# Optimization experiments

Hardware: AMD Instinct MI355X
Metric: run time of the kernel (lower is better)

Reference implementation:

```python
import jax, jax.numpy as jnp
import numpy as np

B, D, N, H, K = 8192, 1024, 4096, 8, 4
T, DECAY, STEPS = 100.0, 0.001, 3


def setup_inputs() -> dict:
    key = jax.random.key(0)
    ks = jax.random.split(key, 16)
    rn = lambda k, sh, s=0.02: jax.random.normal(k, sh, jnp.float32) * s
    return {
        'query': jax.random.normal(ks[0], (B, D), jnp.float32),
        'wm': jax.random.normal(ks[1], (B, D), jnp.float32),
        'keys': jax.random.normal(ks[2], (N, D), jnp.float32) * 0.1,
        'values': jax.random.normal(ks[3], (N, D), jnp.float32) * 0.1,
        'last_access': jax.random.uniform(ks[4], (N,), jnp.float32) * T,
        'importance': jnp.ones((N,), jnp.float32),
        'consolid': jnp.ones((N,), jnp.float32),
        'emo_tags': jax.random.uniform(ks[5], (N, 8), jnp.float32),
        'active': jnp.ones((N,), jnp.float32),
        'in_proj_w': rn(ks[6], (3 * D, D)), 'in_proj_b': jnp.zeros((3 * D,), jnp.float32),
        'out_w': rn(ks[7], (D, D)), 'out_b': jnp.zeros((D,), jnp.float32),
        'msg_w1': rn(ks[8], (D, 2 * D)), 'msg_b1': jnp.zeros((D,), jnp.float32),
        'msg_ln_g': jnp.ones((D,), jnp.float32), 'msg_ln_b': jnp.zeros((D,), jnp.float32),
        'msg_w2': rn(ks[9], (D, D)), 'msg_b2': jnp.zeros((D,), jnp.float32),
        'gru_wih': rn(ks[10], (3 * D, D)), 'gru_whh': rn(ks[11], (3 * D, D)),
        'gru_bih': jnp.zeros((3 * D,), jnp.float32), 'gru_bhh': jnp.zeros((3 * D,), jnp.float32),
        'rsn_w1': rn(ks[12], (D, D)), 'rsn_b1': jnp.zeros((D,), jnp.float32),
        'rsn_ln_g': jnp.ones((D,), jnp.float32), 'rsn_ln_b': jnp.zeros((D,), jnp.float32),
        'rsn_w2': rn(ks[13], (D, D)), 'rsn_b2': jnp.zeros((D,), jnp.float32),
        'top_k': K,
    }


def _ln(x, g, b):
    m = x.mean(-1, keepdims=True)
    v = ((x - m) ** 2).mean(-1, keepdims=True)
    return (x - m) / jnp.sqrt(v + 1e-5) * g + b


def reference(query, wm, keys, values, last_access, importance, consolid, emo_tags, active,
              in_proj_w, in_proj_b, out_w, out_b,
              msg_w1, msg_b1, msg_ln_g, msg_ln_b, msg_w2, msg_b2,
              gru_wih, gru_whh, gru_bih, gru_bhh,
              rsn_w1, rsn_b1, rsn_ln_g, rsn_ln_b, rsn_w2, rsn_b2, top_k):
    sg = jax.lax.stop_gradient
    # --- schema retrieve: cosine sim + forgetting-decay + boosts + topk softmax gather ---
    qn = query / jnp.maximum(jnp.linalg.norm(query, axis=-1, keepdims=True), 1e-8)
    kn = keys / jnp.maximum(jnp.linalg.norm(keys, axis=-1, keepdims=True), 1e-8)
    sims = qn @ kn.T  # [B, N]
    forget = sg(jnp.exp(-DECAY * (T - last_access)))
    boost = sg(emo_tags.sum(-1) * 0.1 + importance * 0.2 + jnp.log1p(consolid) * 0.1)
    scores = (sims * forget + boost) * sg(active)
    top_s, top_i = jax.lax.top_k(scores, top_k)  # [B, K]
    w = jax.nn.softmax(top_s, axis=-1)
    schema = jnp.einsum('bk,bkd->bd', w, values[top_i])  # [B, D]

    # --- GraphReasoner: 3 steps of 2-token MHA + msg_net + GRUCell ---
    dh = D // H
    scale = 1.0 / np.sqrt(dh).astype(np.float32)

    def mha(x):  # x [B, 2, D]
        qkv = x @ in_proj_w.T + in_proj_b
        q, k, v = jnp.split(qkv, 3, axis=-1)
        q = q.reshape(-1, 2, H, dh); k = k.reshape(-1, 2, H, dh); v = v.reshape(-1, 2, H, dh)
        a = jax.nn.softmax(jnp.einsum('bqhd,bkhd->bhqk', q, k) * scale, axis=-1)
        o = jnp.einsum('bhqk,bkhd->bqhd', a, v).reshape(-1, 2, D)
        return o @ out_w.T + out_b

    def gru(x, h):
        gi = x @ gru_wih.T + gru_bih
        gh = h @ gru_whh.T + gru_bhh
        ir, iz, inn = jnp.split(gi, 3, axis=-1)
        hr, hz, hn = jnp.split(gh, 3, axis=-1)
        r = jax.nn.sigmoid(ir + hr)
        z = jax.nn.sigmoid(iz + hz)
        n = jnp.tanh(inn + r * hn)
        return (1.0 - z) * n + z * h

    state = wm
    for _ in range(STEPS):
        ctx = jnp.stack([state, schema], axis=1)  # [B, 2, D]
        att = mha(ctx)
        combined = jnp.concatenate([att[:, 0], att[:, 1]], axis=-1)  # [B, 2D]
        msg = jax.nn.relu(_ln(combined @ msg_w1.T + msg_b1, msg_ln_g, msg_ln_b)) @ msg_w2.T + msg_b2
        state = gru(msg, state)
    out = jax.nn.relu(_ln(state @ rsn_w1.T + rsn_b1, rsn_ln_g, rsn_ln_b)) @ rsn_w2.T + rsn_b2
    return out
```

## Files before the change

kernel.cpp:

```cpp
#include <hip/hip_runtime.h>
#include <cstdint>
#include <cstddef>

typedef __attribute__((ext_vector_type(8))) short short8;
typedef __attribute__((ext_vector_type(4))) float f32x4;
typedef __attribute__((ext_vector_type(4))) unsigned short us4;

#define DEVINL static __device__ __forceinline__
#define AS1 __attribute__((address_space(1)))
#define AS3 __attribute__((address_space(3)))

DEVINL float bf2f(unsigned short u){
  union { unsigned uu; float f; } v; v.uu = ((unsigned)u) << 16; return v.f;
}
DEVINL unsigned short f2bf(float f){
  unsigned u = __float_as_uint(f);
  u += 0x7fffu + ((u >> 16) & 1u);
  return (unsigned short)(u >> 16);
}

DEVINL bool tk_better(float av, int ai, float bv, int bi){
  return (av > bv) || (av == bv && ai < bi);
}
DEVINL void tk_cmpex(float& va, int& ia, float& vb, int& ib){
  if (!tk_better(va, ia, vb, ib)){
    float tv = va; va = vb; vb = tv;
    int t = ia; ia = ib; ib = t;
  }
}
DEVINL void tk_sort4(float* v, int* id){
  tk_cmpex(v[0], id[0], v[1], id[1]);
  tk_cmpex(v[2], id[2], v[3], id[3]);
  tk_cmpex(v[0], id[0], v[2], id[2]);
  tk_cmpex(v[1], id[1], v[3], id[3]);
  tk_cmpex(v[1], id[1], v[2], id[2]);
}
DEVINL void tk_bmerge(float* v, int* id, const float* pv, const int* pi){
  #pragma unroll
  for (int i = 0; i < 4; ++i){
    bool ta = tk_better(v[i], id[i], pv[3 - i], pi[3 - i]);
    v[i]  = ta ? v[i]  : pv[3 - i];
    id[i] = ta ? id[i] : pi[3 - i];
  }
  tk_cmpex(v[0], id[0], v[2], id[2]);
  tk_cmpex(v[1], id[1], v[3], id[3]);
  tk_cmpex(v[0], id[0], v[1], id[1]);
  tk_cmpex(v[2], id[2], v[3], id[3]);
}

__global__ void k_diag(float* out, float v){ out[0] = v; }

__global__ __launch_bounds__(256) void k_cast_bf16(const float* __restrict__ x,
                                                   unsigned short* __restrict__ y, int n4){
  int stride = gridDim.x * blockDim.x;
  for (int i = blockIdx.x * blockDim.x + threadIdx.x; i < n4; i += stride){
    float4 v = ((const float4*)x)[i];
    us4 o; o[0] = f2bf(v.x); o[1] = f2bf(v.y); o[2] = f2bf(v.z); o[3] = f2bf(v.w);
    ((us4*)y)[i] = o;
  }
}

__global__ __launch_bounds__(256) void k_tcast(const float* __restrict__ in,
    unsigned short* __restrict__ outT, int R, int C){
  __shared__ float t[32][33];
  const int bc = blockIdx.x * 32, br = blockIdx.y * 32;
  const int lx = threadIdx.x & 31, ly = threadIdx.x >> 5;
  #pragma unroll
  for (int i = 0; i < 32; i += 8)
    t[ly + i][lx] = in[(size_t)(br + ly + i) * C + bc + lx];
  __syncthreads();
  #pragma unroll
  for (int i = 0; i < 32; i += 8)
    outT[(size_t)(bc + ly + i) * R + br + lx] = f2bf(t[lx][ly + i]);
}

__global__ __launch_bounds__(256) void k_bias_pre(const float* __restrict__ w1,
    const float* __restrict__ outb, const float* __restrict__ b1, float* __restrict__ bc){
  int wave = threadIdx.x >> 6, lane = threadIdx.x & 63;
  int j = blockIdx.x * 4 + wave;
  float s = 0.f;
  for (int m = lane; m < 2048; m += 64)
    s += w1[(size_t)j * 2048 + m] * outb[m & 1023];
  #pragma unroll
  for (int m = 32; m >= 1; m >>= 1) s += __shfl_xor(s, m);
  if (lane == 0) bc[j] = s + b1[j];
}

__global__ __launch_bounds__(256) void k_bias_gi(const float* __restrict__ wih,
    const float* __restrict__ b2, const float* __restrict__ bih, float* __restrict__ bc){
  int wave = threadIdx.x >> 6, lane = threadIdx.x & 63;
  int n = blockIdx.x * 4 + wave;
  float s = 0.f;
  for (int m = lane; m < 1024; m += 64)
    s += wih[(size_t)n * 1024 + m] * b2[m];
  #pragma unroll
  for (int m = 32; m >= 1; m >>= 1) s += __shfl_xor(s, m);
  if (lane == 0) bc[n] = s + bih[n];
}

__global__ __launch_bounds__(256) void k_prep_keys(const float* __restrict__ keys,
    const float* __restrict__ last_access, const float* __restrict__ importance,
    const float* __restrict__ consolid, const float* __restrict__ emo,
    const float* __restrict__ active, float* __restrict__ ascale, float* __restrict__ bbias){
  int wave = threadIdx.x >> 6, lane = threadIdx.x & 63;
  int n = blockIdx.x * 4 + wave;
  const float* kr = keys + (size_t)n * 1024;
  float s = 0.f;
  #pragma unroll
  for (int j = 0; j < 4; ++j){
    float4 v = ((const float4*)kr)[j * 64 + lane];
    s += v.x*v.x + v.y*v.y + v.z*v.z + v.w*v.w;
  }
  #pragma unroll
  for (int m = 32; m >= 1; m >>= 1) s += __shfl_xor(s, m);
  if (lane == 0){
    float norm = fmaxf(sqrtf(s), 1e-8f);
    float forget = expf(-0.001f * (100.0f - last_access[n]));
    float bo = 0.f;
    #pragma unroll
    for (int j = 0; j < 8; ++j) bo += emo[n * 8 + j];
    bo = bo * 0.1f + importance[n] * 0.2f + log1pf(consolid[n]) * 0.1f;
    float a = active[n];
    ascale[n] = forget * a / norm;
    bbias[n]  = bo * a;
  }
}

__global__ __launch_bounds__(256) void k_qnorm(const float* __restrict__ q, float* __restrict__ qinv){
  int wave = threadIdx.x >> 6, lane = threadIdx.x & 63;
  int b = blockIdx.x * 4 + wave;
  const float* qr = q + (size_t)b * 1024;
  float s = 0.f;
  #pragma unroll
  for (int j = 0; j < 4; ++j){
    float4 v = ((const float4*)qr)[j * 64 + lane];
    s += v.x*v.x + v.y*v.y + v.z*v.z + v.w*v.w;
  }
  #pragma unroll
  for (int m = 32; m >= 1; m >>= 1) s += __shfl_xor(s, m);
  if (lane == 0) qinv[b] = 1.0f / fmaxf(sqrtf(s), 1e-8f);
}

__global__ __launch_bounds__(256) void k_split(const float* __restrict__ X,
    const float* __restrict__ rscale, unsigned short* __restrict__ Hi,
    unsigned short* __restrict__ Lo){
  const int row = blockIdx.x;
  const float sc = rscale ? rscale[row] : 1.0f;
  const int d = threadIdx.x * 4;
  float4 v = *(const float4*)(X + (size_t)row * 1024 + d);
  float xs[4] = {v.x * sc, v.y * sc, v.z * sc, v.w * sc};
  us4 h, l;
  #pragma unroll
  for (int j = 0; j < 4; ++j){
    unsigned short hb = f2bf(xs[j]);
    h[j] = hb;
    l[j] = f2bf(xs[j] - bf2f(hb));
  }
  *(us4*)(Hi + (size_t)row * 1024 + d) = h;
  *(us4*)(Lo + (size_t)row * 1024 + d) = l;
}

__global__ __launch_bounds__(256) void k_scores_mfma(
    const unsigned short* __restrict__ Qhi, const unsigned short* __restrict__ Qlo,
    const unsigned short* __restrict__ Khi, const unsigned short* __restrict__ Klo,
    const float* __restrict__ ascale, const float* __restrict__ bbias,
    float* __restrict__ candV, int* __restrict__ candI){
  __shared__ __align__(16) unsigned short AsH[128 * 32];
  __shared__ __align__(16) unsigned short AsL[128 * 32];
  __shared__ __align__(16) unsigned short BsH[128 * 32];
  __shared__ __align__(16) unsigned short BsL[128 * 32];
  const int tid = threadIdx.x;
  const int wave = tid >> 6, lane = tid & 63;
  const int tM = blockIdx.x, tN = blockIdx.y;
  const int wm_ = wave >> 1, wn_ = wave & 1;
  f32x4 acc[4][4] = {};
  const unsigned short* AH = Qhi + (size_t)tM * 128 * 1024;
  const unsigned short* AL = Qlo + (size_t)tM * 128 * 1024;
  const unsigned short* BH = Khi + (size_t)tN * 128 * 1024;
  const unsigned short* BL = Klo + (size_t)tN * 128 * 1024;
  const int lrow = lane & 15, lk = (lane >> 4) * 8;
  for (int k0 = 0; k0 < 1024; k0 += 32){
    __syncthreads();
    #pragma unroll
    for (int j = 0; j < 2; ++j){
      int c = wave * 128 + j * 64 + lane;
      int row = c >> 2, cp = c & 3;
      size_t go = (size_t)row * 1024 + k0 + cp * 8;
      int lo_ = (wave * 2 + j) * 512;
      __builtin_amdgcn_global_load_lds((const AS1 void*)(AH + go), (AS3 void*)(AsH + lo_), 16, 0, 0);
      __builtin_amdgcn_global_load_lds((const AS1 void*)(AL + go), (AS3 void*)(AsL + lo_), 16, 0, 0);
      __builtin_amdgcn_global_load_lds((const AS1 void*)(BH + go), (AS3 void*)(BsH + lo_), 16, 0, 0);
      __builtin_amdgcn_global_load_lds((const AS1 void*)(BL + go), (AS3 void*)(BsL + lo_), 16, 0, 0);
    }
    __syncthreads();
    short8 ah[4], al[4], bh[4], bl[4];
    #pragma unroll
    for (int mi = 0; mi < 4; ++mi){
      int ro = (wm_ * 64 + mi * 16 + lrow) * 32 + lk;
      ah[mi] = *(const short8*)(AsH + ro);
      al[mi] = *(const short8*)(AsL + ro);
    }
    #pragma unroll
    for (int ni = 0; ni < 4; ++ni){
      int ro = (wn_ * 64 + ni * 16 + lrow) * 32 + lk;
      bh[ni] = *(const short8*)(BsH + ro);
      bl[ni] = *(const short8*)(BsL + ro);
    }
    #pragma unroll
    for (int mi = 0; mi < 4; ++mi)
      #pragma unroll
      for (int ni = 0; ni < 4; ++ni){
        acc[mi][ni] = __builtin_amdgcn_mfma_f32_16x16x32_bf16(ah[mi], bh[ni], acc[mi][ni], 0, 0, 0);
        acc[mi][ni] = __builtin_amdgcn_mfma_f32_16x16x32_bf16(ah[mi], bl[ni], acc[mi][ni], 0, 0, 0);
        acc[mi][ni] = __builtin_amdgcn_mfma_f32_16x16x32_bf16(al[mi], bh[ni], acc[mi][ni], 0, 0, 0);
      }
  }
  const int lc = lane & 15;
  float as_[4], bb_[4]; int cid[4];
  #pragma unroll
  for (int ni = 0; ni < 4; ++ni){
    cid[ni] = tN * 128 + wn_ * 64 + ni * 16 + lc;
    as_[ni] = ascale[cid[ni]];
    bb_[ni] = bbias[cid[ni]];
  }
  #pragma unroll
  for (int mi = 0; mi < 4; ++mi){
    #pragma unroll
    for (int r = 0; r < 4; ++r){
      float v[4]; int id[4];
      #pragma unroll
      for (int ni = 0; ni < 4; ++ni){
        v[ni]  = acc[mi][ni][r] * as_[ni] + bb_[ni];
        id[ni] = cid[ni];
      }
      tk_sort4(v, id);
      #pragma unroll
      for (int mask = 1; mask <= 8; mask <<= 1){
        float pv[4]; int pi_[4];
        #pragma unroll
        for (int j = 0; j < 4; ++j){
          pv[j]  = __shfl_xor(v[j], mask);
          pi_[j] = __shfl_xor(id[j], mask);
        }
        tk_bmerge(v, id, pv, pi_);
      }
      if (lc == 0){
        int row = tM * 128 + wm_ * 64 + mi * 16 + (lane >> 4) * 4 + r;
        size_t cb = (size_t)row * 256 + tN * 8 + wn_ * 4;
        #pragma unroll
        for (int j = 0; j < 4; ++j){ candV[cb + j] = v[j]; candI[cb + j] = id[j]; }
      }
    }
  }
}

__global__ __launch_bounds__(256) void k_topk_merge(const float* __restrict__ candV,
    const int* __restrict__ candI, const float* __restrict__ V,
    unsigned short* __restrict__ schema_bf){
  const int row = blockIdx.x, tid = threadIdx.x;
  const int wave = tid >> 6, lane = tid & 63;
  float v[4]; int id[4];
  v[0] = candV[(size_t)row * 256 + tid];
  id[0] = candI[(size_t)row * 256 + tid];
  #pragma unroll
  for (int j = 1; j < 4; ++j){ v[j] = -3.4e38f; id[j] = 0x7fffffff; }
  #pragma unroll
  for (int mask = 1; mask <= 32; mask <<= 1){
    float pv[4]; int pi_[4];
    #pragma unroll
    for (int j = 0; j < 4; ++j){
      pv[j]  = __shfl_xor(v[j], mask);
      pi_[j] = __shfl_xor(id[j], mask);
    }
    tk_bmerge(v, id, pv, pi_);
  }
  __shared__ float wv[4][4]; __shared__ int wi[4][4];
  if (lane == 0){
    #pragma unroll
    for (int j = 0; j < 4; ++j){ wv[wave][j] = v[j]; wi[wave][j] = id[j]; }
  }
  __syncthreads();
  __shared__ float w_sh[4]; __shared__ int i_sh[4];
  if (tid == 0){
    float fv[4]; int fi[4];
    #pragma unroll
    for (int j = 0; j < 4; ++j){ fv[j] = wv[0][j]; fi[j] = wi[0][j]; }
    #pragma unroll
    for (int w = 1; w < 4; ++w){
      float pv[4]; int pi_[4];
      #pragma unroll
      for (int j = 0; j < 4; ++j){ pv[j] = wv[w][j]; pi_[j] = wi[w][j]; }
      tk_bmerge(fv, fi, pv, pi_);
    }
    float m = fv[0];
    float e0 = expf(fv[0] - m), e1 = expf(fv[1] - m), e2 = expf(fv[2] - m), e3 = expf(fv[3] - m);
    float inv = 1.f / (e0 + e1 + e2 + e3);
    w_sh[0] = e0 * inv; w_sh[1] = e1 * inv; w_sh[2] = e2 * inv; w_sh[3] = e3 * inv;
    i_sh[0] = fi[0]; i_sh[1] = fi[1]; i_sh[2] = fi[2]; i_sh[3] = fi[3];
  }
  __syncthreads();
  float w0 = w_sh[0], w1 = w_sh[1], w2 = w_sh[2], w3 = w_sh[3];
  const float* v0 = V + (size_t)i_sh[0] * 1024;
  const float* v1 = V + (size_t)i_sh[1] * 1024;
  const float* v2 = V + (size_t)i_sh[2] * 1024;
  const float* v3 = V + (size_t)i_sh[3] * 1024;
  int d = tid * 4;
  float4 a = *(const float4*)(v0 + d);
  float4 b4 = *(const float4*)(v1 + d);
  float4 c = *(const float4*)(v2 + d);
  float4 e = *(const float4*)(v3 + d);
  us4 o;
  o[0] = f2bf(w0*a.x + w1*b4.x + w2*c.x + w3*e.x);
  o[1] = f2bf(w0*a.y + w1*b4.y + w2*c.y + w3*e.y);
  o[2] = f2bf(w0*a.z + w1*b4.z + w2*c.z + w3*e.z);
  o[3] = f2bf(w0*a.w + w1*b4.w + w2*c.w + w3*e.w);
  *(us4*)(schema_bf + (size_t)row * 1024 + d) = o;
}

__global__ __launch_bounds__(256) void k_initstate(const float* __restrict__ wm,
    float* __restrict__ st, unsigned short* __restrict__ stbf){
  size_t i = ((size_t)blockIdx.x * 256 + threadIdx.x) * 4;
  float4 v = *(const float4*)(wm + i);
  *(float4*)(st + i) = v;
  us4 o; o[0] = f2bf(v.x); o[1] = f2bf(v.y); o[2] = f2bf(v.z); o[3] = f2bf(v.w);
  *(us4*)(stbf + i) = o;
}

template<int OUT_BF16>
__global__ __launch_bounds__(256) void k_gemm(const unsigned short* __restrict__ A,
    const unsigned short* __restrict__ W, const float* __restrict__ bias,
    void* __restrict__ C, int M, int N, int K, int lda, int ldc){
  __shared__ __align__(16) unsigned short As[128 * 32];
  __shared__ __align__(16) unsigned short Ws[128 * 32];
  const int tid = threadIdx.x;
  const int wave = tid >> 6, lane = tid & 63;
  const int tM = blockIdx.x, tN = blockIdx.y;
  const int wm_ = wave >> 1, wn_ = wave & 1;
  f32x4 acc[4][4] = {};
  const unsigned short* Abase = A + (size_t)tM * 128 * lda;
  const unsigned short* Wbase = W + (size_t)tN * 128 * K;
  const int lrow = lane & 15, lk = (lane >> 4) * 8;
  for (int k0 = 0; k0 < K; k0 += 32){
    __syncthreads();
    #pragma unroll
    for (int j = 0; j < 2; ++j){
      int c = wave * 128 + j * 64 + lane;
      int row = c >> 2, cp = c & 3;
      const unsigned short* ga = Abase + (size_t)row * lda + k0 + cp * 8;
      const unsigned short* gw = Wbase + (size_t)row * K + k0 + cp * 8;
      __builtin_amdgcn_global_load_lds((const AS1 void*)ga, (AS3 void*)(As + (wave * 2 + j) * 512), 16, 0, 0);
      __builtin_amdgcn_global_load_lds((const AS1 void*)gw, (AS3 void*)(Ws + (wave * 2 + j) * 512), 16, 0, 0);
    }
    __syncthreads();
    short8 af[4], bfr[4];
    #pragma unroll
    for (int mi = 0; mi < 4; ++mi)
      af[mi] = *(const short8*)(As + (wm_ * 64 + mi * 16 + lrow) * 32 + lk);
    #pragma unroll
    for (int ni = 0; ni < 4; ++ni)
      bfr[ni] = *(const short8*)(Ws + (wn_ * 64 + ni * 16 + lrow) * 32 + lk);
    #pragma unroll
    for (int mi = 0; mi < 4; ++mi)
      #pragma unroll
      for (int ni = 0; ni < 4; ++ni)
        acc[mi][ni] = __builtin_amdgcn_mfma_f32_16x16x32_bf16(af[mi], bfr[ni], acc[mi][ni], 0, 0, 0);
  }
  const int lc = lane & 15, lr = (lane >> 4) * 4;
  #pragma unroll
  for (int ni = 0; ni < 4; ++ni){
    int col = tN * 128 + wn_ * 64 + ni * 16 + lc;
    float bb = bias ? bias[col] : 0.f;
    #pragma unroll
    for (int mi = 0; mi < 4; ++mi){
      int rowb = tM * 128 + wm_ * 64 + mi * 16 + lr;
      #pragma unroll
      for (int r = 0; r < 4; ++r){
        float vv = acc[mi][ni][r] + bb;
        size_t off = (size_t)(rowb + r) * ldc + col;
        if (OUT_BF16) ((unsigned short*)C)[off] = f2bf(vv);
        else ((float*)C)[off] = vv;
      }
    }
  }
}

DEVINL int chunk_swz(int q){ return (q & ~7) | ((q & 7) ^ ((q >> 3) & 7)); }

template<int OUT_BF16>
__global__ __launch_bounds__(512, 2) void k_gemm256(const unsigned short* __restrict__ A,
    const unsigned short* __restrict__ W, const float* __restrict__ bias,
    void* __restrict__ C, int M, int N, int K, int lda, int ldc){
  __shared__ __align__(16) unsigned short lds[65536];
  const int tid = threadIdx.x;
  const int wave = tid >> 6, lane = tid & 63;
  const int wr = wave >> 2, wc = wave & 3;
  const int lrow = lane & 15, lkk = lane >> 4;

  const int nwg = gridDim.x * gridDim.y;
  int lin = blockIdx.y * gridDim.x + blockIdx.x;
  int cpx = nwg >> 3;
  int swz = (lin & 7) * cpx + (lin >> 3);
  const int nM = M >> 8;
  const int tM = swz % nM, tN = swz / nM;

  const unsigned short* Abase = A + (size_t)tM * 256 * lda;
  const unsigned short* Wbase = W + (size_t)tN * 256 * K;

  f32x4 acc[8][4] = {};

  auto STAGE = [&](int kt, int buf){
    const int k0 = kt * 64;
    #pragma unroll
    for (int j = 0; j < 4; ++j){
      int qst = j * 512 + tid;
      int g = chunk_swz(qst);
      int row = g >> 3, c = g & 7;
      int dst = buf * 32768 + (j * 512 + wave * 64) * 8;
      __builtin_amdgcn_global_load_lds((const AS1 void*)(Abase + (size_t)row * lda + k0 + c * 8),
          (AS3 void*)(lds + dst), 16, 0, 0);
      __builtin_amdgcn_global_load_lds((const AS1 void*)(Wbase + (size_t)row * K + k0 + c * 8),
          (AS3 void*)(lds + 16384 + dst), 16, 0, 0);
    }
  };

  const int ntiles = K >> 6;
  STAGE(0, 0);
  if (ntiles > 1) STAGE(1, 1);

  for (int t = 0; t < ntiles; ++t){
    const int cur = t & 1;
    if (t + 1 < ntiles) asm volatile("s_waitcnt vmcnt(8)" ::: "memory");
    else                asm volatile("s_waitcnt vmcnt(0)" ::: "memory");
    __builtin_amdgcn_s_barrier();
    __builtin_amdgcn_sched_barrier(0);
    const int ab = cur * 32768, bb = cur * 32768 + 16384;
    #pragma unroll
    for (int mh = 0; mh < 2; ++mh){
      short8 af[4][2];
      #pragma unroll
      for (int mi = 0; mi < 4; ++mi)
        #pragma unroll
        for (int kk = 0; kk < 2; ++kk){
          int q = (wr * 128 + (mh * 4 + mi) * 16 + lrow) * 8 + kk * 4 + lkk;
          af[mi][kk] = *(const short8*)(lds + ab + chunk_swz(q) * 8);
        }
      #pragma unroll
      for (int nh = 0; nh < 2; ++nh){
        short8 bf[2][2];
        #pragma unroll
        for (int ni = 0; ni < 2; ++ni)
          #pragma unroll
          for (int kk = 0; kk < 2; ++kk){
            int q = (wc * 64 + (nh * 2 + ni) * 16 + lrow) * 8 + kk * 4 + lkk;
            bf[ni][kk] = *(const short8*)(lds + bb + chunk_swz(q) * 8);
          }
        __builtin_amdgcn_s_setprio(1);
        #pragma unroll
        for (int mi = 0; mi < 4; ++mi)
          #pragma unroll
          for (int ni = 0; ni < 2; ++ni)
            #pragma unroll
            for (int kk = 0; kk < 2; ++kk)
              acc[mh * 4 + mi][nh * 2 + ni] =
                __builtin_amdgcn_mfma_f32_16x16x32_bf16(af[mi][kk], bf[ni][kk],
                                                        acc[mh * 4 + mi][nh * 2 + ni], 0, 0, 0);
        __builtin_amdgcn_s_setprio(0);
      }
    }
    __builtin_amdgcn_sched_barrier(0);
    __builtin_amdgcn_s_barrier();
    if (t + 2 < ntiles) STAGE(t + 2, cur);
  }

  const int lc = lane & 15, lr = (lane >> 4) * 4;
  #pragma unroll
  for (int ni = 0; ni < 4; ++ni){
    int col = tN * 256 + wc * 64 + ni * 16 + lc;
    float bb2 = bias ? bias[col] : 0.f;
    #pragma unroll
    for (int mi = 0; mi < 8; ++mi){
      int rowb = tM * 256 + wr * 128 + mi * 16 + lr;
      #pragma unroll
      for (int r = 0; r < 4; ++r){
        float vv = acc[mi][ni][r] + bb2;
        size_t off = (size_t)(rowb + r) * ldc + col;
        if (OUT_BF16) ((unsigned short*)C)[off] = f2bf(vv);
        else ((float*)C)[off] = vv;
      }
    }
  }
}

__global__ __launch_bounds__(256) void k_attn(const unsigned short* __restrict__ qkvS,
    const unsigned short* __restrict__ qkvM, unsigned short* __restrict__ catt){
  const int b = blockIdx.x, tid = threadIdx.x;
  const int l = tid & 31;
  const int e = (tid >> 5) * 128 + l * 4;
  const unsigned short* ps = qkvS + (size_t)b * 3072;
  const unsigned short* pm = qkvM + (size_t)b * 3072;
  float q0[4], kk0[4], v0[4], q1[4], kk1[4], v1[4];
  us4 t;
  t = *(const us4*)(ps + e);        for (int j = 0; j < 4; ++j) q0[j]  = bf2f(t[j]);
  t = *(const us4*)(ps + 1024 + e); for (int j = 0; j < 4; ++j) kk0[j] = bf2f(t[j]);
  t = *(const us4*)(ps + 2048 + e); for (int j = 0; j < 4; ++j) v0[j]  = bf2f(t[j]);
  t = *(const us4*)(pm + e);        for (int j = 0; j < 4; ++j) q1[j]  = bf2f(t[j]);
  t = *(const us4*)(pm + 1024 + e); for (int j = 0; j < 4; ++j) kk1[j] = bf2f(t[j]);
  t = *(const us4*)(pm + 2048 + e); for (int j = 0; j < 4; ++j) v1[j]  = bf2f(t[j]);
  float s00 = 0.f, s01 = 0.f, s10 = 0.f, s11 = 0.f;
  #pragma unroll
  for (int j = 0; j < 4; ++j){
    s00 += q0[j] * kk0[j]; s01 += q0[j] * kk1[j];
    s10 += q1[j] * kk0[j]; s11 += q1[j] * kk1[j];
  }
  #pragma unroll
  for (int m = 16; m >= 1; m >>= 1){
    s00 += __shfl_xor(s00, m); s01 += __shfl_xor(s01, m);
    s10 += __shfl_xor(s10, m); s11 += __shfl_xor(s11, m);
  }
  const float sc = 0.08838834764831845f;
  s00 *= sc; s01 *= sc; s10 *= sc; s11 *= sc;
  float m0 = fmaxf(s00, s01), m1 = fmaxf(s10, s11);
  float e00 = expf(s00 - m0), e01 = expf(s01 - m0);
  float e10 = expf(s10 - m1), e11 = expf(s11 - m1);
  float i0 = 1.f / (e00 + e01), i1 = 1.f / (e10 + e11);
  float w00 = e00 * i0, w01 = e01 * i0, w10 = e10 * i1, w11 = e11 * i1;
  us4 o0, o1;
  #pragma unroll
  for (int j = 0; j < 4; ++j){
    o0[j] = f2bf(w00 * v0[j] + w01 * v1[j]);
    o1[j] = f2bf(w10 * v0[j] + w11 * v1[j]);
  }
  *(us4*)(catt + (size_t)b * 2048 + e)        = o0;
  *(us4*)(catt + (size_t)b * 2048 + 1024 + e) = o1;
}

__global__ __launch_bounds__(256) void k_ln_relu(const float* __restrict__ X,
    const float* __restrict__ g, const float* __restrict__ bta, unsigned short* __restrict__ Y){
  const int row = blockIdx.x, tid = threadIdx.x;
  const float* x = X + (size_t)row * 1024;
  const int d = tid * 4;
  float4 v = *(const float4*)(x + d);
  float s1 = v.x + v.y + v.z + v.w;
  float s2 = v.x*v.x + v.y*v.y + v.z*v.z + v.w*v.w;
  #pragma unroll
  for (int m = 32; m >= 1; m >>= 1){ s1 += __shfl_xor(s1, m); s2 += __shfl_xor(s2, m); }
  __shared__ float a1[4], a2[4];
  int wave = tid >> 6, lane = tid & 63;
  if (lane == 0){ a1[wave] = s1; a2[wave] = s2; }
  __syncthreads();
  s1 = a1[0] + a1[1] + a1[2] + a1[3];
  s2 = a2[0] + a2[1] + a2[2] + a2[3];
  float mean = s1 * (1.f / 1024.f);
  float var  = s2 * (1.f / 1024.f) - mean * mean;
  float rstd = rsqrtf(var + 1e-5f);
  float4 gg = *(const float4*)(g + d);
  float4 bb = *(const float4*)(bta + d);
  us4 o;
  o[0] = f2bf(fmaxf((v.x - mean) * rstd * gg.x + bb.x, 0.f));
  o[1] = f2bf(fmaxf((v.y - mean) * rstd * gg.y + bb.y, 0.f));
  o[2] = f2bf(fmaxf((v.z - mean) * rstd * gg.z + bb.z, 0.f));
  o[3] = f2bf(fmaxf((v.w - mean) * rstd * gg.w + bb.w, 0.f));
  *(us4*)(Y + (size_t)row * 1024 + d) = o;
}

__global__ __launch_bounds__(256) void k_gru(const unsigned short* __restrict__ gi,
    const unsigned short* __restrict__ gh, const float* __restrict__ h,
    float* __restrict__ hn, unsigned short* __restrict__ hnbf){
  const int b = blockIdx.x;
  const int d = threadIdx.x * 4;
  const unsigned short* pi = gi + (size_t)b * 3072;
  const unsigned short* ph = gh + (size_t)b * 3072;
  us4 t;
  float ir[4], iz[4], in_[4], hr[4], hz[4], hnn[4];
  t = *(const us4*)(pi + d);        for (int j = 0; j < 4; ++j) ir[j]  = bf2f(t[j]);
  t = *(const us4*)(pi + 1024 + d); for (int j = 0; j < 4; ++j) iz[j]  = bf2f(t[j]);
  t = *(const us4*)(pi + 2048 + d); for (int j = 0; j < 4; ++j) in_[j] = bf2f(t[j]);
  t = *(const us4*)(ph + d);        for (int j = 0; j < 4; ++j) hr[j]  = bf2f(t[j]);
  t = *(const us4*)(ph + 1024 + d); for (int j = 0; j < 4; ++j) hz[j]  = bf2f(t[j]);
  t = *(const us4*)(ph + 2048 + d); for (int j = 0; j < 4; ++j) hnn[j] = bf2f(t[j]);
  float4 hv = *(const float4*)(h + (size_t)b * 1024 + d);
  float hvv[4] = {hv.x, hv.y, hv.z, hv.w};
  float ov[4]; us4 ob;
  #pragma unroll
  for (int j = 0; j < 4; ++j){
    float r = 1.f / (1.f + expf(-(ir[j] + hr[j])));
    float z = 1.f / (1.f + expf(-(iz[j] + hz[j])));
    float n = tanhf(in_[j] + r * hnn[j]);
    float o = (1.f - z) * n + z * hvv[j];
    ov[j] = o; ob[j] = f2bf(o);
  }
  float4 of; of.x = ov[0]; of.y = ov[1]; of.z = ov[2]; of.w = ov[3];
  *(float4*)(hn + (size_t)b * 1024 + d) = of;
  *(us4*)(hnbf + (size_t)b * 1024 + d) = ob;
}

extern "C" void kernel_launch(void* const* d_in, const int* in_sizes, int n_in,
                              void* d_out, int out_size, void* d_ws, size_t ws_size,
                              hipStream_t stream) {
  (void)in_sizes; (void)n_in; (void)out_size;
  const float* query       = (const float*)d_in[0];
  const float* wm          = (const float*)d_in[1];
  const float* keys        = (const float*)d_in[2];
  const float* values      = (const float*)d_in[3];
  const float* last_access = (const float*)d_in[4];
  const float* importance  = (const float*)d_in[5];
  const float* consolid    = (const float*)d_in[6];
  const float* emo         = (const float*)d_in[7];
  const float* active      = (const float*)d_in[8];
  const float* in_proj_w   = (const float*)d_in[9];
  const float* in_proj_b   = (const float*)d_in[10];
  const float* out_w       = (const float*)d_in[11];
  const float* out_b       = (const float*)d_in[12];
  const float* msg_w1      = (const float*)d_in[13];
  const float* msg_b1      = (const float*)d_in[14];
  const float* msg_ln_g    = (const float*)d_in[15];
  const float* msg_ln_b    = (const float*)d_in[16];
  const float* msg_w2      = (const float*)d_in[17];
  const float* msg_b2      = (const float*)d_in[18];
  const float* gru_wih     = (const float*)d_in[19];
  const float* gru_whh     = (const float*)d_in[20];
  const float* gru_bih     = (const float*)d_in[21];
  const float* gru_bhh     = (const float*)d_in[22];
  const float* rsn_w1      = (const float*)d_in[23];
  const float* rsn_b1      = (const float*)d_in[24];
  const float* rsn_ln_g    = (const float*)d_in[25];
  const float* rsn_ln_b    = (const float*)d_in[26];
  const float* rsn_w2      = (const float*)d_in[27];
  const float* rsn_b2      = (const float*)d_in[28];
  float* out = (float*)d_out;

  size_t off = 0;
  char* base = (char*)d_ws;
  auto carve = [&](size_t bytes) -> char* {
    char* p = base + off;
    off += (bytes + 255) & ~(size_t)255;
    return p;
  };
  float* ascale = (float*)carve(4096*4);
  float* bbias  = (float*)carve(4096*4);
  float* qinv   = (float*)carve(8192*4);
  float* bc_pre = (float*)carve(1024*4);
  float* bc_gi  = (float*)carve(3072*4);
  unsigned short* wb_inproj = (unsigned short*)carve((size_t)3072*1024*2);
  unsigned short* wb_gwhh   = (unsigned short*)carve((size_t)3072*1024*2);
  unsigned short* wb_rw1    = (unsigned short*)carve((size_t)1024*1024*2);
  unsigned short* wb_rw2    = (unsigned short*)carve((size_t)1024*1024*2);
  unsigned short* wb_Wab    = (unsigned short*)carve((size_t)1024*2048*2);
  unsigned short* wb_Wc     = (unsigned short*)carve((size_t)3072*1024*2);
  unsigned short* schema_bf = (unsigned short*)carve((size_t)8192*1024*2);
  float*          state_f   = (float*)carve((size_t)8192*1024*4);
  unsigned short* state_bf  = (unsigned short*)carve((size_t)8192*1024*2);
  unsigned short* qkvM      = (unsigned short*)carve((size_t)8192*3072*2);
  unsigned short* bufP      = (unsigned short*)carve((size_t)8192*3072*2);
  unsigned short* bufQ      = (unsigned short*)carve((size_t)8192*3072*2);

  if (off > ws_size){
    k_diag<<<1, 1, 0, stream>>>(out, (float)(ws_size >> 20));
    return;
  }

  unsigned short* tmp_w1bf  = bufQ;
  unsigned short* tmp_outwT = bufQ + (size_t)1024*2048;
  unsigned short* tmp_w2T   = tmp_outwT + (size_t)1024*1024;
  unsigned short* tmp_wihbf = tmp_w2T + (size_t)1024*1024;

  unsigned short* Qhi = qkvM;
  unsigned short* Qlo = Qhi + (size_t)8192*1024;
  unsigned short* Khi = Qlo + (size_t)8192*1024;
  unsigned short* Klo = Khi + (size_t)4096*1024;
  float* candV = (float*)bufP;
  int*   candI = (int*)((char*)bufP + (size_t)8192*256*4);

  unsigned short* qkvS  = bufP;
  unsigned short* catt  = bufQ;
  float*          preln = (float*)bufP;
  unsigned short* h1buf = bufQ;
  unsigned short* gibuf = bufP;
  unsigned short* ghbuf = bufQ;

  auto cast = [&](const float* src, unsigned short* dst, int n){
    k_cast_bf16<<<1024, 256, 0, stream>>>(src, dst, n / 4);
  };
  cast(in_proj_w, wb_inproj, 3072*1024);
  cast(gru_whh,   wb_gwhh,   3072*1024);
  cast(rsn_w1,    wb_rw1,    1024*1024);
  cast(rsn_w2,    wb_rw2,    1024*1024);
  cast(msg_w1,    tmp_w1bf,  1024*2048);
  cast(gru_wih,   tmp_wihbf, 3072*1024);
  k_tcast<<<dim3(32, 32), 256, 0, stream>>>(out_w,  tmp_outwT, 1024, 1024);
  k_tcast<<<dim3(32, 32), 256, 0, stream>>>(msg_w2, tmp_w2T,   1024, 1024);
  k_bias_pre<<<256, 256, 0, stream>>>(msg_w1, out_b, msg_b1, bc_pre);
  k_bias_gi<<<768, 256, 0, stream>>>(gru_wih, msg_b2, gru_bih, bc_gi);
  k_gemm<1><<<dim3(8, 8), 256, 0, stream>>>(tmp_w1bf,        tmp_outwT, nullptr, wb_Wab,        1024, 1024, 1024, 2048, 2048);
  k_gemm<1><<<dim3(8, 8), 256, 0, stream>>>(tmp_w1bf + 1024, tmp_outwT, nullptr, wb_Wab + 1024, 1024, 1024, 1024, 2048, 2048);
  k_gemm<1><<<dim3(24, 8), 256, 0, stream>>>(tmp_wihbf, tmp_w2T, nullptr, wb_Wc, 3072, 1024, 1024, 1024, 1024);

  k_qnorm<<<2048, 256, 0, stream>>>(query, qinv);
  k_prep_keys<<<1024, 256, 0, stream>>>(keys, last_access, importance, consolid, emo, active, ascale, bbias);
  k_split<<<8192, 256, 0, stream>>>(query, qinv, Qhi, Qlo);
  k_split<<<4096, 256, 0, stream>>>(keys, nullptr, Khi, Klo);
  k_scores_mfma<<<dim3(64, 32), 256, 0, stream>>>(Qhi, Qlo, Khi, Klo, ascale, bbias, candV, candI);
  k_topk_merge<<<8192, 256, 0, stream>>>(candV, candI, values, schema_bf);

  k_initstate<<<8192, 256, 0, stream>>>(wm, state_f, state_bf);
  k_gemm256<1><<<dim3(32, 12), 512, 0, stream>>>(schema_bf, wb_inproj, in_proj_b, qkvM, 8192, 3072, 1024, 1024, 3072);
  for (int s = 0; s < 3; ++s){
    k_gemm256<1><<<dim3(32, 12), 512, 0, stream>>>(state_bf, wb_inproj, in_proj_b, qkvS, 8192, 3072, 1024, 1024, 3072);
    k_attn<<<8192, 256, 0, stream>>>(qkvS, qkvM, catt);
    k_gemm<0><<<dim3(64, 8), 256, 0, stream>>>(catt, wb_Wab, bc_pre, preln, 8192, 1024, 2048, 2048, 1024);
    k_ln_relu<<<8192, 256, 0, stream>>>(preln, msg_ln_g, msg_ln_b, h1buf);
    k_gemm256<1><<<dim3(32, 12), 512, 0, stream>>>(h1buf, wb_Wc, bc_gi, gibuf, 8192, 3072, 1024, 1024, 3072);
    k_gemm256<1><<<dim3(32, 12), 512, 0, stream>>>(state_bf, wb_gwhh, gru_bhh, ghbuf, 8192, 3072, 1024, 1024, 3072);
    k_gru<<<8192, 256, 0, stream>>>(gibuf, ghbuf, state_f, state_f, state_bf);
  }
  k_gemm<0><<<dim3(64, 8), 256, 0, stream>>>(state_bf, wb_rw1, rsn_b1, (float*)bufP, 8192, 1024, 1024, 1024, 1024);
  k_ln_relu<<<8192, 256, 0, stream>>>((float*)bufP, rsn_ln_g, rsn_ln_b, bufQ);
  k_gemm<0><<<dim3(64, 8), 256, 0, stream>>>(bufQ, wb_rw2, rsn_b2, out, 8192, 1024, 1024, 1024, 1024);
}
```

Before: 1.698 ms.

## Rewrite 256x256 GEMM as 8-phase pipeline with half-tile staging

Replaces the double-buffered 256-tile GEMM with an 8-phase schedule. Each half-tile of A and B (128 rows) is loaded and staged separately, and its MFMAs are interleaved with the global-to-LDS loads for the next tiles. Four quadrant accumulators are computed in turn, with barriers between phases, so memory traffic overlaps with compute at a finer grain. The many barriers add sync overhead. Correctness depends on the intricate slot/half reuse ordering and assumes an even tile count.

```diff
diff --git a/kernel.cpp b/kernel.cpp
--- a/kernel.cpp
+++ b/kernel.cpp
@@ -384,16 +384,14 @@
   }
 }
 
-DEVINL int chunk_swz(int q){ return (q & ~7) | ((q & 7) ^ ((q >> 3) & 7)); }
-
 template<int OUT_BF16>
-__global__ __launch_bounds__(512, 2) void k_gemm256(const unsigned short* __restrict__ A,
+__global__ __launch_bounds__(512, 2) void k_gemm8p(const unsigned short* __restrict__ A,
     const unsigned short* __restrict__ W, const float* __restrict__ bias,
     void* __restrict__ C, int M, int N, int K, int lda, int ldc){
   __shared__ __align__(16) unsigned short lds[65536];
   const int tid = threadIdx.x;
   const int wave = tid >> 6, lane = tid & 63;
-  const int wr = wave >> 2, wc = wave & 3;
+  const int wqr = wave >> 2, wqc = wave & 3;
   const int lrow = lane & 15, lkk = lane >> 4;
 
   const int nwg = gridDim.x * gridDim.y;
@@ -406,89 +404,121 @@
   const unsigned short* Abase = A + (size_t)tM * 256 * lda;
   const unsigned short* Wbase = W + (size_t)tN * 256 * K;
 
-  f32x4 acc[8][4] = {};
-
-  auto STAGE = [&](int kt, int buf){
-    const int k0 = kt * 64;
-    #pragma unroll
-    for (int j = 0; j < 4; ++j){
-      int qst = j * 512 + tid;
-      int g = chunk_swz(qst);
-      int row = g >> 3, c = g & 7;
-      int dst = buf * 32768 + (j * 512 + wave * 64) * 8;
-      __builtin_amdgcn_global_load_lds((const AS1 void*)(Abase + (size_t)row * lda + k0 + c * 8),
-          (AS3 void*)(lds + dst), 16, 0, 0);
-      __builtin_amdgcn_global_load_lds((const AS1 void*)(Wbase + (size_t)row * K + k0 + c * 8),
-          (AS3 void*)(lds + 16384 + dst), 16, 0, 0);
+  f32x4 a00[4][2] = {}, a01[4][2] = {}, a11[4][2] = {}, a10[4][2] = {};
+  short8 af[4][2], bf[2][2];
+  const int ntiles = K >> 6;
+
+  auto stage = [&](int op, int slot, int half, int tile){
+    if (tile >= ntiles) return;
+    const unsigned short* G = op ? Wbase : Abase;
+    const int rs = op ? K : lda;
+    const int k0 = tile * 64, hr = half * 128;
+    const int base = op * 32768 + slot * 16384 + half * 8192;
+    #pragma unroll
+    for (int l = 0; l < 2; ++l){
+      int p = l * 512 + tid;
+      int row = p >> 3, c = (p & 7) ^ (row & 7);
+      int dstc = l * 512 + wave * 64;
+      __builtin_amdgcn_global_load_lds(
+          (const AS1 void*)(G + (size_t)(hr + row) * rs + k0 + c * 8),
+          (AS3 void*)(lds + base + dstc * 8), 16, 0, 0);
     }
   };
-
-  const int ntiles = K >> 6;
-  STAGE(0, 0);
-  if (ntiles > 1) STAGE(1, 1);
-
-  for (int t = 0; t < ntiles; ++t){
-    const int cur = t & 1;
-    if (t + 1 < ntiles) asm volatile("s_waitcnt vmcnt(8)" ::: "memory");
-    else                asm volatile("s_waitcnt vmcnt(0)" ::: "memory");
+  auto ldA = [&](int slot, int half){
+    const int base = slot * 16384 + half * 8192;
+    #pragma unroll
+    for (int mi = 0; mi < 4; ++mi)
+      #pragma unroll
+      for (int kk = 0; kk < 2; ++kk){
+        int row = wqr * 64 + mi * 16 + lrow;
+        int c = kk * 4 + lkk;
+        af[mi][kk] = *(const short8*)(lds + base + (row * 8 + (c ^ (row & 7))) * 8);
+      }
+  };
+  auto ldB = [&](int slot, int half){
+    const int base = 32768 + slot * 16384 + half * 8192;
+    #pragma unroll
+    for (int ni = 0; ni < 2; ++ni)
+      #pragma unroll
+      for (int kk = 0; kk < 2; ++kk){
+        int row = wqc * 32 + ni * 16 + lrow;
+        int c = kk * 4 + lkk;
+        bf[ni][kk] = *(const short8*)(lds + base + (row * 8 + (c ^ (row & 7))) * 8);
+      }
+  };
+  auto mfma16 = [&](f32x4 (&acc)[4][2]){
+    __builtin_amdgcn_s_setprio(1);
+    #pragma unroll
+    for (int mi = 0; mi < 4; ++mi)
+      #pragma unroll
+      for (int ni = 0; ni < 2; ++ni)
+        #pragma unroll
+        for (int kk = 0; kk < 2; ++kk)
+          acc[mi][ni] = __builtin_amdgcn_mfma_f32_16x16x32_bf16(af[mi][kk], bf[ni][kk], acc[mi][ni], 0, 0, 0);
+    __builtin_amdgcn_s_setprio(0);
+  };
+  auto SB = [&](){
+    __builtin_amdgcn_sched_barrier(0);
     __builtin_amdgcn_s_barrier();
     __builtin_amdgcn_sched_barrier(0);
-    const int ab = cur * 32768, bb = cur * 32768 + 16384;
-    #pragma unroll
-    for (int mh = 0; mh < 2; ++mh){
-      short8 af[4][2];
-      #pragma unroll
-      for (int mi = 0; mi < 4; ++mi)
+  };
+
+  stage(0,0,0, 0); stage(1,0,0, 0); stage(1,0,1, 0); stage(0,0,1, 0);
+  stage(0,1,0, 1); stage(1,1,1, 1);
+  __builtin_amdgcn_sched_barrier(0);
+  asm volatile("s_waitcnt vmcnt(4)" ::: "memory");
+  __builtin_amdgcn_s_barrier();
+  __builtin_amdgcn_sched_barrier(0);
+
+  for (int j = 0; j < (ntiles >> 1); ++j){
+    const int t0 = 2 * j;
+    ldA(0,0); ldB(0,0); stage(0,1,1, t0+1);
+    SB(); mfma16(a00); SB();
+    ldB(0,1); stage(1,1,0, t0+1);
+    SB(); mfma16(a01); SB();
+    ldA(0,1); stage(0,0,0, t0+2);
+    SB(); mfma16(a11); SB();
+    ldB(0,0); stage(1,0,1, t0+2);
+    SB(); mfma16(a10);
+    __builtin_amdgcn_sched_barrier(0);
+    if (t0 + 2 < ntiles) asm volatile("s_waitcnt vmcnt(4)" ::: "memory");
+    else                 asm volatile("s_waitcnt vmcnt(0)" ::: "memory");
+    __builtin_amdgcn_s_barrier();
+    __builtin_amdgcn_sched_barrier(0);
+    ldA(1,0); ldB(1,0); stage(0,0,1, t0+2);
+    SB(); mfma16(a00); SB();
+    ldB(1,1); stage(1,0,0, t0+2);
+    SB(); mfma16(a01); SB();
+    ldA(1,1); stage(0,1,0, t0+3);
+    SB(); mfma16(a11); SB();
+    ldB(1,0); stage(1,1,1, t0+3);
+    SB(); mfma16(a10);
+    __builtin_amdgcn_sched_barrier(0);
+    asm volatile("s_waitcnt vmcnt(4)" ::: "memory");
+    __builtin_amdgcn_s_barrier();
+    __builtin_amdgcn_sched_barrier(0);
+  }
+
+  const int lc = lane & 15, lr = (lane >> 4) * 4;
+  auto wout = [&](f32x4 (&acc)[4][2], int MH, int NH){
+    #pragma unroll
+    for (int ni = 0; ni < 2; ++ni){
+      int col = tN * 256 + NH * 128 + wqc * 32 + ni * 16 + lc;
+      float bb = bias ? bias[col] : 0.f;
+      #pragma unroll
+      for (int mi = 0; mi < 4; ++mi){
+        int rowb = tM * 256 + MH * 128 + wqr * 64 + mi * 16 + lr;
         #pragma unroll
-        for (int kk = 0; kk < 2; ++kk){
-          int q = (wr * 128 + (mh * 4 + mi) * 16 + lrow) * 8 + kk * 4 + lkk;
-          af[mi][kk] = *(const short8*)(lds + ab + chunk_swz(q) * 8);
+        for (int r = 0; r < 4; ++r){
+          float vv = acc[mi][ni][r] + bb;
+          size_t off = (size_t)(rowb + r) * ldc + col;
+          if (OUT_BF16) ((unsigned short*)C)[off] = f2bf(vv);
+          else ((float*)C)[off] = vv;
         }
-      #pragma unroll
-      for (int nh = 0; nh < 2; ++nh){
-        short8 bf[2][2];
-        #pragma unroll
-        for (int ni = 0; ni < 2; ++ni)
-          #pragma unroll
-          for (int kk = 0; kk < 2; ++kk){
-            int q = (wc * 64 + (nh * 2 + ni) * 16 + lrow) * 8 + kk * 4 + lkk;
-            bf[ni][kk] = *(const short8*)(lds + bb + chunk_swz(q) * 8);
-          }
-        __builtin_amdgcn_s_setprio(1);
-        #pragma unroll
-        for (int mi = 0; mi < 4; ++mi)
-          #pragma unroll
-          for (int ni = 0; ni < 2; ++ni)
-            #pragma unroll
-            for (int kk = 0; kk < 2; ++kk)
-              acc[mh * 4 + mi][nh * 2 + ni] =
-                __builtin_amdgcn_mfma_f32_16x16x32_bf16(af[mi][kk], bf[ni][kk],
-                                                        acc[mh * 4 + mi][nh * 2 + ni], 0, 0, 0);
-        __builtin_amdgcn_s_setprio(0);
       }
     }
-    __builtin_amdgcn_sched_barrier(0);
-    __builtin_amdgcn_s_barrier();
-    if (t + 2 < ntiles) STAGE(t + 2, cur);
-  }
-
-  const int lc = lane & 15, lr = (lane >> 4) * 4;
-  #pragma unroll
-  for (int ni = 0; ni < 4; ++ni){
-    int col = tN * 256 + wc * 64 + ni * 16 + lc;
-    float bb2 = bias ? bias[col] : 0.f;
-    #pragma unroll
-    for (int mi = 0; mi < 8; ++mi){
-      int rowb = tM * 256 + wr * 128 + mi * 16 + lr;
-      #pragma unroll
-      for (int r = 0; r < 4; ++r){
-        float vv = acc[mi][ni][r] + bb2;
-        size_t off = (size_t)(rowb + r) * ldc + col;
-        if (OUT_BF16) ((unsigned short*)C)[off] = f2bf(vv);
-        else ((float*)C)[off] = vv;
-      }
-    }
-  }
+  };
+  wout(a00, 0, 0); wout(a01, 0, 1); wout(a11, 1, 1); wout(a10, 1, 0);
 }
 
 __global__ __launch_bounds__(256) void k_attn(const unsigned short* __restrict__ qkvS,
@@ -703,14 +733,14 @@
   k_topk_merge<<<8192, 256, 0, stream>>>(candV, candI, values, schema_bf);
 
   k_initstate<<<8192, 256, 0, stream>>>(wm, state_f, state_bf);
-  k_gemm256<1><<<dim3(32, 12), 512, 0, stream>>>(schema_bf, wb_inproj, in_proj_b, qkvM, 8192, 3072, 1024, 1024, 3072);
+  k_gemm8p<1><<<dim3(32, 12), 512, 0, stream>>>(schema_bf, wb_inproj, in_proj_b, qkvM, 8192, 3072, 1024, 1024, 3072);
   for (int s = 0; s < 3; ++s){
-    k_gemm256<1><<<dim3(32, 12), 512, 0, stream>>>(state_bf, wb_inproj, in_proj_b, qkvS, 8192, 3072, 1024, 1024, 3072);
+    k_gemm8p<1><<<dim3(32, 12), 512, 0, stream>>>(state_bf, wb_inproj, in_proj_b, qkvS, 8192, 3072, 1024, 1024, 3072);
     k_attn<<<8192, 256, 0, stream>>>(qkvS, qkvM, catt);
     k_gemm<0><<<dim3(64, 8), 256, 0, stream>>>(catt, wb_Wab, bc_pre, preln, 8192, 1024, 2048, 2048, 1024);
     k_ln_relu<<<8192, 256, 0, stream>>>(preln, msg_ln_g, msg_ln_b, h1buf);
-    k_gemm256<1><<<dim3(32, 12), 512, 0, stream>>>(h1buf, wb_Wc, bc_gi, gibuf, 8192, 3072, 1024, 1024, 3072);
-    k_gemm256<1><<<dim3(32, 12), 512, 0, stream>>>(state_bf, wb_gwhh, gru_bhh, ghbuf, 8192, 3072, 1024, 1024, 3072);
+    k_gemm8p<1><<<dim3(32, 12), 512, 0, stream>>>(h1buf, wb_Wc, bc_gi, gibuf, 8192, 3072, 1024, 1024, 3072);
+    k_gemm8p<1><<<dim3(32, 12), 512, 0, stream>>>(state_bf, wb_gwhh, gru_bhh, ghbuf, 8192, 3072, 1024, 1024, 3072);
     k_gru<<<8192, 256, 0, stream>>>(gibuf, ghbuf, state_f, state_f, state_bf);
   }
   k_gemm<0><<<dim3(64, 8), 256, 0, stream>>>(state_bf, wb_rw1, rsn_b1, (float*)bufP, 8192, 1024, 1024, 1024, 1024);
```

New measurement: 1.564 ms. 1.09x faster.
